# Performance work log

Measured on AMD Instinct MI355X. Metric: run time of the kernel, lower is better.

## Reference

```python
import jax, jax.numpy as jnp
import numpy as np
from jax import lax

EMBED_DIM = 512
HIDDEN_DIM = 256
OUT_DIM = HIDDEN_DIM // 2
BATCH = 32
SEQ = 4096
THRESHOLD = 1.0
DECAY = 0.95
REFRACTORY = 2.0


def setup_inputs() -> dict:
    key = jax.random.key(0)
    k1, k2, k3 = jax.random.split(key, 3)
    x = jax.random.normal(k1, (BATCH, SEQ, EMBED_DIM), dtype=jnp.float32)
    input_weights = jax.random.normal(k2, (EMBED_DIM, HIDDEN_DIM), dtype=jnp.float32) * 0.1
    hidden_weights = jax.random.normal(k3, (HIDDEN_DIM, OUT_DIM), dtype=jnp.float32) * 0.1
    return {"x": x, "input_weights": input_weights, "hidden_weights": hidden_weights}


def reference(x, input_weights, hidden_weights):
    B, S, D = x.shape
    H = input_weights.shape[1]
    dt = x.dtype
    # batch-mean then project all timesteps at once: [S, H]
    currents = jnp.einsum('sd,dh->sh', x.mean(0), input_weights)

    def step(carry, ic):
        mem, refr = carry
        active = (refr <= 0).astype(dt)
        mem = DECAY * mem + ic * active
        spikes = (mem >= THRESHOLD).astype(dt)
        mem = mem * (1.0 - spikes)
        refr = jnp.maximum(refr - 1.0, 0.0) + spikes * REFRACTORY
        return (mem, refr), spikes

    init = (jnp.zeros((H,), dt), jnp.zeros((H,), dt))
    _, spikes = lax.scan(step, init, currents)  # spikes: [S, H]
    out = spikes @ hidden_weights               # [S, OUT]
    out_mean = out.mean(0)                      # mean over timesteps
    # original repeats the (batch-independent) output across the batch
    return jnp.broadcast_to(out_mean, (B, out_mean.shape[0]))
```

## Files before the change

kernel.cpp:

```cpp
#include <hip/hip_runtime.h>
#include <stdint.h>


#define S_LEN 4096
#define D_DIM 512
#define H_DIM 256
#define O_DIM 128
#define B_SZ  32

#define NPROD 1024
#define NCONS 4
#define CH    64
#define NCH   (S_LEN / CH)
#define NGRP  16
#define GOAL  64u

#define LIF_STEP(IC) {                          \
    float ict = sp2 ? 0.f : (IC);               \
    float tt  = fmaf(0.95f, u, ict);            \
    u   = sp1 ? 0.f : tt;                       \
    bool sp = (u >= 1.0f);                      \
    cnt += sp ? 1 : 0;                          \
    sp2 = sp1; sp1 = sp; }

#define ACC4(A, V) { A.x += V.x; A.y += V.y; A.z += V.z; A.w += V.w; }

#define CISSUE(BUF, C) {                                                     \
    const float* p_ = csrc + (size_t)(C) * (CH * H_DIM);                     \
    _Pragma("unroll")                                                        \
    for (int r_ = 0; r_ < CH; ++r_)                                          \
        BUF[r_] = __hip_atomic_load(p_ + (size_t)r_ * H_DIM,                 \
                                    __ATOMIC_RELAXED,                        \
                                    __HIP_MEMORY_SCOPE_AGENT);              \
    __builtin_amdgcn_sched_barrier(0); }

#define CSCAN(BUF) {                                                         \
    _Pragma("unroll")                                                        \
    for (int r_ = 0; r_ < CH; ++r_) { LIF_STEP(BUF[r_]); }                   \
    __builtin_amdgcn_sched_barrier(0); }

__global__ __launch_bounds__(256, 2)
void snn_fused(const float4* __restrict__ x4,
               const float*  __restrict__ iw,
               const float*  __restrict__ hw,
               float*        __restrict__ cur,
               uint32_t*     __restrict__ ctr,
               float*        __restrict__ out) {
    __shared__ __attribute__((aligned(16))) char smem[4 * 128 * 16 + 256];
    const int t = threadIdx.x;

    if (blockIdx.x >= NCONS) {
        float4* xm = (float4*)smem;
        const int r2 = t >> 7;
        const int d4 = t & 127;
        const int h  = t;
        const float inv = 1.0f / (float)B_SZ;
        const size_t bstr = (size_t)S_LEN * (D_DIM / 4);

        const int f  = (int)blockIdx.x - NCONS;
        const int s0 = 4 * f;

        float4 a0 = make_float4(0.f, 0.f, 0.f, 0.f);
        float4 a1 = make_float4(0.f, 0.f, 0.f, 0.f);
        const float4* xb = x4 + (size_t)(s0 + r2) * (D_DIM / 4) + d4;
        for (int b = 0; b < B_SZ; b += 4) {
            const float4* p = xb + (size_t)b * bstr;
            float4 v00 = p[0],            v01 = p[2 * (D_DIM / 4)];
            float4 v10 = p[bstr],         v11 = p[bstr + 2 * (D_DIM / 4)];
            float4 v20 = p[2 * bstr],     v21 = p[2 * bstr + 2 * (D_DIM / 4)];
            float4 v30 = p[3 * bstr],     v31 = p[3 * bstr + 2 * (D_DIM / 4)];
            ACC4(a0, v00); ACC4(a0, v10); ACC4(a0, v20); ACC4(a0, v30);
            ACC4(a1, v01); ACC4(a1, v11); ACC4(a1, v21); ACC4(a1, v31);
        }
        a0.x *= inv; a0.y *= inv; a0.z *= inv; a0.w *= inv;
        a1.x *= inv; a1.y *= inv; a1.z *= inv; a1.w *= inv;
        xm[r2 * (D_DIM / 4) + d4]       = a0;
        xm[(r2 + 2) * (D_DIM / 4) + d4] = a1;
        __syncthreads();

        float acc2[4] = {0.f, 0.f, 0.f, 0.f};
        for (int d4i = 0; d4i < D_DIM / 4; ++d4i) {
            const int d = d4i * 4;
            float w0 = iw[(d + 0) * H_DIM + h];
            float w1 = iw[(d + 1) * H_DIM + h];
            float w2 = iw[(d + 2) * H_DIM + h];
            float w3 = iw[(d + 3) * H_DIM + h];
            #pragma unroll
            for (int r = 0; r < 4; ++r) {
                float4 xv = xm[r * (D_DIM / 4) + d4i];
                acc2[r] += xv.x * w0 + xv.y * w1 + xv.z * w2 + xv.w * w3;
            }
        }
        {
            float* dst = cur + (size_t)s0 * H_DIM + h;
            #pragma unroll
            for (int r = 0; r < 4; ++r)
                __hip_atomic_store(dst + (size_t)r * H_DIM, acc2[r],
                                   __ATOMIC_RELAXED, __HIP_MEMORY_SCOPE_AGENT);
        }
        __syncthreads();
        if (t == 0)
            __hip_atomic_fetch_add(&ctr[f >> 6], 1u, __ATOMIC_RELAXED,
                                   __HIP_MEMORY_SCOPE_AGENT);
        return;
    }

    if (t >= 64) return;
    float* cl = (float*)(smem + 4 * 128 * 16);
    const int lane  = t;
    const int hbase = (int)blockIdx.x * 64;
    const float* csrc = cur + hbase + lane;

    auto wait_grp = [&](int c) {
        if ((c & 3) != 0) return;
        const int gi = c >> 2;
        if (lane == 0) {
            while (__hip_atomic_load(&ctr[gi], __ATOMIC_RELAXED,
                                     __HIP_MEMORY_SCOPE_AGENT) < GOAL)
                __builtin_amdgcn_s_sleep(8);
        }
    };

    float va[CH], vb[CH];
    float u = 0.f;
    int   cnt = 0;
    bool  sp1 = false, sp2 = false;

    wait_grp(0);
    CISSUE(va, 0);
    for (int c = 0; c < NCH; c += 2) {
        CISSUE(vb, c + 1);
        CSCAN(va);
        if (c + 2 < NCH) {
            wait_grp(c + 2);
            CISSUE(va, c + 2);
        }
        CSCAN(vb);
    }

    __syncthreads();
    cl[lane] = (float)cnt;
    __syncthreads();
    float a0 = 0.f, a1 = 0.f;
    #pragma unroll 8
    for (int k = 0; k < 64; ++k) {
        float c = cl[k];
        const float* w = hw + (size_t)(hbase + k) * O_DIM;
        a0 = fmaf(c, w[lane], a0);
        a1 = fmaf(c, w[lane + 64], a1);
    }
    a0 *= (1.0f / (float)S_LEN);
    a1 *= (1.0f / (float)S_LEN);
    for (int b = 0; b < B_SZ; ++b) {
        atomicAdd(out + b * O_DIM + lane,      a0);
        atomicAdd(out + b * O_DIM + lane + 64, a1);
    }
}

extern "C" void kernel_launch(void* const* d_in, const int* in_sizes, int n_in,
                              void* d_out, int out_size, void* d_ws, size_t ws_size,
                              hipStream_t stream) {
    const float4* x4 = (const float4*)d_in[0];
    const float*  iw = (const float*) d_in[1];
    const float*  hw = (const float*) d_in[2];
    float* out = (float*)d_out;
    float* cur = (float*)d_ws;
    uint32_t* ctr = (uint32_t*)((char*)d_ws + (size_t)4 * 1024 * 1024);

    (void)hipMemsetAsync(ctr, 0, NGRP * sizeof(uint32_t), stream);
    (void)hipMemsetAsync(out, 0, B_SZ * O_DIM * sizeof(float), stream);
    hipLaunchKernelGGL(snn_fused, dim3(NCONS + NPROD), dim3(256), 0, stream,
                       x4, iw, hw, cur, ctr, out);
}
```

Before: 448.4 us.

## Stage currents into LDS via async global_load_lds with timestep-interleaved float4 layout

Producers now write the four timesteps of each hidden unit contiguously, as a float4 per (group, h), instead of row-major [S,H]. Consumers stage each 64-step chunk into a double-buffered LDS region with global_load_lds 16-byte async copies, wait with an explicit vmcnt, then read float4s back and run the LIF scan. This replaces 64 scalar atomic loads per chunk with 16 wide loads and frees a large register buffer on the serial consumer path. The risks are whether relaxed-visibility semantics still hold for the async LDS loads, and that the hand-written vmcnt(16) assumes exact instruction counts.

After: 474.9 us. +5.9%, slower.

```diff
diff --git a/kernel.cpp b/kernel.cpp
--- a/kernel.cpp
+++ b/kernel.cpp
@@ -12,8 +12,12 @@
 #define NCONS 4
 #define CH    64
 #define NCH   (S_LEN / CH)
+#define ROWS  (CH / 4)
 #define NGRP  16
 #define GOAL  64u
+
+typedef const __attribute__((address_space(1))) void  glob_void;
+typedef       __attribute__((address_space(3))) void  lds_void;
 
 #define LIF_STEP(IC) {                          \
     float ict = sp2 ? 0.f : (IC);               \
@@ -25,20 +29,6 @@
 
 #define ACC4(A, V) { A.x += V.x; A.y += V.y; A.z += V.z; A.w += V.w; }
 
-#define CISSUE(BUF, C) {                                                     \
-    const float* p_ = csrc + (size_t)(C) * (CH * H_DIM);                     \
-    _Pragma("unroll")                                                        \
-    for (int r_ = 0; r_ < CH; ++r_)                                          \
-        BUF[r_] = __hip_atomic_load(p_ + (size_t)r_ * H_DIM,                 \
-                                    __ATOMIC_RELAXED,                        \
-                                    __HIP_MEMORY_SCOPE_AGENT);              \
-    __builtin_amdgcn_sched_barrier(0); }
-
-#define CSCAN(BUF) {                                                         \
-    _Pragma("unroll")                                                        \
-    for (int r_ = 0; r_ < CH; ++r_) { LIF_STEP(BUF[r_]); }                   \
-    __builtin_amdgcn_sched_barrier(0); }
-
 __global__ __launch_bounds__(256, 2)
 void snn_fused(const float4* __restrict__ x4,
                const float*  __restrict__ iw,
@@ -46,7 +36,7 @@
                float*        __restrict__ cur,
                uint32_t*     __restrict__ ctr,
                float*        __restrict__ out) {
-    __shared__ __attribute__((aligned(16))) char smem[4 * 128 * 16 + 256];
+    __shared__ __attribute__((aligned(16))) char smem[2 * ROWS * 64 * 16 + 256];
     const int t = threadIdx.x;
 
     if (blockIdx.x >= NCONS) {
@@ -92,10 +82,10 @@
             }
         }
         {
-            float* dst = cur + (size_t)s0 * H_DIM + h;
+            float* dst = cur + ((size_t)f * H_DIM + h) * 4;
             #pragma unroll
             for (int r = 0; r < 4; ++r)
-                __hip_atomic_store(dst + (size_t)r * H_DIM, acc2[r],
+                __hip_atomic_store(dst + r, acc2[r],
                                    __ATOMIC_RELAXED, __HIP_MEMORY_SCOPE_AGENT);
         }
         __syncthreads();
@@ -106,10 +96,11 @@
     }
 
     if (t >= 64) return;
-    float* cl = (float*)(smem + 4 * 128 * 16);
+    float4 (*lbuf)[ROWS * 64] = (float4 (*)[ROWS * 64])smem;
+    float* cl = (float*)(smem + 2 * ROWS * 64 * 16);
     const int lane  = t;
     const int hbase = (int)blockIdx.x * 64;
-    const float* csrc = cur + hbase + lane;
+    const float4* cur4 = (const float4*)cur;
 
     auto wait_grp = [&](int c) {
         if ((c & 3) != 0) return;
@@ -120,22 +111,41 @@
                 __builtin_amdgcn_s_sleep(8);
         }
     };
+    auto stage = [&](int c) {
+        #pragma unroll
+        for (int r = 0; r < ROWS; ++r) {
+            const float4* g = cur4 + (size_t)(c * ROWS + r) * H_DIM + hbase + lane;
+            __builtin_amdgcn_global_load_lds((glob_void*)g,
+                                             (lds_void*)&lbuf[c & 1][r * 64 + lane],
+                                             16, 0, 0);
+        }
+    };
 
-    float va[CH], vb[CH];
     float u = 0.f;
     int   cnt = 0;
     bool  sp1 = false, sp2 = false;
 
     wait_grp(0);
-    CISSUE(va, 0);
-    for (int c = 0; c < NCH; c += 2) {
-        CISSUE(vb, c + 1);
-        CSCAN(va);
-        if (c + 2 < NCH) {
-            wait_grp(c + 2);
-            CISSUE(va, c + 2);
+    stage(0);
+    for (int c = 0; c < NCH; ++c) {
+        if (c + 1 < NCH) {
+            wait_grp(c + 1);
+            stage(c + 1);
+            asm volatile("s_waitcnt vmcnt(16)" ::: "memory");
+        } else {
+            asm volatile("s_waitcnt vmcnt(0)" ::: "memory");
         }
-        CSCAN(vb);
+        __builtin_amdgcn_sched_barrier(0);
+        const float4* lb = lbuf[c & 1];
+        float4 v[ROWS];
+        #pragma unroll
+        for (int r = 0; r < ROWS; ++r) v[r] = lb[r * 64 + lane];
+        __builtin_amdgcn_sched_barrier(0);
+
+        #pragma unroll
+        for (int r = 0; r < ROWS; ++r) {
+            LIF_STEP(v[r].x); LIF_STEP(v[r].y); LIF_STEP(v[r].z); LIF_STEP(v[r].w);
+        }
     }
 
     __syncthreads();
```
